# Kernel tuning notes

Measured on AMD Instinct MI355X. Metric: run time of the kernel, lower is better.

## Reference

```python
import jax, jax.numpy as jnp
import numpy as np

PAD = 4
B, C, H, W = 64, 9, 256, 256


def setup_inputs() -> dict:
    key = jax.random.key(0)
    k1, k2, k3 = jax.random.split(key, 3)
    x = jax.random.normal(k1, (B, C, H, W), dtype=jnp.float32)
    shift_x = jax.random.randint(k2, (B,), 0, 2 * PAD + 1, dtype=jnp.int32)
    shift_y = jax.random.randint(k3, (B,), 0, 2 * PAD + 1, dtype=jnp.int32)
    return {"x": x, "shift_x": shift_x, "shift_y": shift_y}


def _lerp_gather(xp, idx_f, axis_size, axis):
    """Separable bilinear tap along one spatial axis with zeros padding.

    xp: (B, C, D2, D3); idx_f: (B, L) fractional pixel indices along `axis`.
    Returns gathered+interpolated tensor with that axis resized to L.
    """
    i0 = jnp.floor(idx_f)
    w1 = idx_f - i0
    w0 = 1.0 - w1
    i1 = i0 + 1.0

    def tap(i, w):
        valid = (i >= 0) & (i <= axis_size - 1)  # zeros padding_mode
        ic = jnp.clip(i, 0, axis_size - 1).astype(jnp.int32)
        wm = w * valid
        if axis == 3:
            g = jnp.take_along_axis(xp, ic[:, None, None, :], axis=3)
            return g * wm[:, None, None, :]
        else:
            g = jnp.take_along_axis(xp, ic[:, None, :, None], axis=2)
            return g * wm[:, None, :, None]

    return tap(i0, w0) + tap(i1, w1)


def reference(x, shift_x, shift_y):
    b, c, h, w = x.shape
    p = PAD
    hp, wp = h + 2 * p, w + 2 * p
    # replicate pad
    x_pad = jnp.pad(x, ((0, 0), (0, 0), (p, p), (p, p)), mode='edge')
    # base grid (normalized coords, H/W points spanning [-1+eps, 1-eps])
    eps_h, eps_w = 2.0 / hp, 2.0 / wp
    gy = jnp.linspace(-1.0 + eps_h, 1.0 - eps_h, h).astype(x.dtype)  # (H,)
    gx = jnp.linspace(-1.0 + eps_w, 1.0 - eps_w, w).astype(x.dtype)  # (W,)
    # per-sample integer-pixel shift in normalized units
    gxb = gx[None, :] + shift_x.astype(x.dtype)[:, None] * (2.0 / wp)  # (B,W)
    gyb = gy[None, :] + shift_y.astype(x.dtype)[:, None] * (2.0 / hp)  # (B,H)
    # normalized -> pixel coords (align_corners=False)
    ix = ((gxb + 1.0) * wp - 1.0) * 0.5  # (B,W)
    iy = ((gyb + 1.0) * hp - 1.0) * 0.5  # (B,H)
    # separable bilinear grid_sample with zeros padding
    tmp = _lerp_gather(x_pad, ix, wp, axis=3)  # (B,C,Hp,W)
    out = _lerp_gather(tmp, iy, hp, axis=2)    # (B,C,H,W)
    return out
```

## Files before the change

kernel.cpp:

```cpp
#include <hip/hip_runtime.h>

#define PAD 4
#define B_ 64
#define C_ 9
#define H_ 256
#define W_ 256
#define PEXT 264
#define TILE_R 16
#define SROWS 18
#define LROW 268
#define NBLK (B_ * C_ * (H_ / TILE_R))

__global__ __launch_bounds__(256) void RandomShiftsAug_kernel(
    const float* __restrict__ x,
    const int* __restrict__ shift_x,
    const int* __restrict__ shift_y,
    float* __restrict__ out)
{
    __shared__ float sm[SROWS * LROW];

    const int tid  = threadIdx.x;
    const int lane = tid & 63;
    const int wv   = tid >> 6;

    const int wid  = (blockIdx.x & 7) * (NBLK / 8) + (blockIdx.x >> 3);

    const int bc   = wid >> 4;
    const int rblk = wid & 15;
    const int i0   = rblk << 4;
    const int b    = bc / C_;

    const float STEP = 262.0f / 255.0f;
    const float sx = (float)shift_x[b];
    const float sy = (float)shift_y[b];
    const float xbase = 0.5f + sx;
    const float ybase = 0.5f + sy;

    const int sr_base = (int)floorf(fmaf((float)i0, STEP, ybase));
    const int sr_last = (int)floorf(fmaf((float)(i0 + TILE_R - 1), STEP, ybase)) + 1;
    const int srows   = sr_last - sr_base + 1;

    const float* __restrict__ plane = x + (size_t)bc * (size_t)(H_ * W_);

    for (int s = wv; s < srows; s += 4) {
        const int rs = min(max(sr_base + s - PAD, 0), H_ - 1);
        const float* src = plane + rs * W_ + lane * 4;
        float* dst = &sm[s * LROW + 4];
        __builtin_amdgcn_global_load_lds(
            (const __attribute__((address_space(1))) void*)src,
            (__attribute__((address_space(3))) void*)dst,
            16, 0, 0);
    }

    if (tid < srows * 9) {
        const int s = tid / 9;
        const int e = tid - s * 9;
        const int rs = min(max(sr_base + s - PAD, 0), H_ - 1);
        const int p    = (e < 4) ? e : (256 + e);
        const int srcc = (e < 4) ? 0 : (W_ - 1);
        sm[s * LROW + p] = plane[rs * W_ + srcc];
    }
    __syncthreads();

    float wx0[4], wx1[4];
    int rdc[4];
    #pragma unroll
    for (int c = 0; c < 4; ++c) {
        const int j   = lane + 64 * c;
        const float ixv = fmaf((float)j, STEP, xbase);
        const float fx  = floorf(ixv);
        const int   px0 = (int)fx;
        float w1 = ixv - fx;
        float w0 = 1.0f - w1;
        if (px0 > PEXT - 1)     w0 = 0.0f;
        if (px0 + 1 > PEXT - 1) w1 = 0.0f;
        wx0[c] = w0;
        wx1[c] = w1;
        rdc[c] = min(px0, PEXT - 1);
    }

    #pragma unroll
    for (int m = 0; m < 4; ++m) {
        const int i = i0 + wv * 4 + m;
        const float iyv = fmaf((float)i, STEP, ybase);
        const float fy  = floorf(iyv);
        const int   py0 = (int)fy;
        float wy1 = iyv - fy;
        float wy0 = 1.0f - wy1;
        if (py0 > PEXT - 1)     wy0 = 0.0f;
        if (py0 + 1 > PEXT - 1) wy1 = 0.0f;
        const int s0 = py0 - sr_base;
        const float* __restrict__ r0p = &sm[s0 * LROW];
        const float* __restrict__ r1p = r0p + LROW;
        float* __restrict__ orow = out + ((size_t)(bc * H_ + i)) * (size_t)W_;

        #pragma unroll
        for (int c = 0; c < 4; ++c) {
            const int rd = rdc[c];
            const float v00 = r0p[rd], v01 = r0p[rd + 1];
            const float v10 = r1p[rd], v11 = r1p[rd + 1];
            const float a0 = fmaf(v00, wx0[c], v01 * wx1[c]);
            const float a1 = fmaf(v10, wx0[c], v11 * wx1[c]);
            orow[lane + 64 * c] = fmaf(a0, wy0, a1 * wy1);
        }
    }
}

extern "C" void kernel_launch(void* const* d_in, const int* in_sizes, int n_in,
                              void* d_out, int out_size, void* d_ws, size_t ws_size,
                              hipStream_t stream) {
    const float* x       = (const float*)d_in[0];
    const int*   shift_x = (const int*)d_in[1];
    const int*   shift_y = (const int*)d_in[2];
    float*       out     = (float*)d_out;

    RandomShiftsAug_kernel<<<NBLK, 256, 0, stream>>>(x, shift_x, shift_y, out);
}
```

Measured before the change: 52.35 us.

## Drop padded LDS halo, fold edge clamping into weights, store float2 outputs

Shared memory rows now hold only the 256 real columns, so the extra scalar pass that filled the replicate-pad halo is removed. The edge behaviour is rebuilt by clamping the column index and moving the weight onto the surviving tap. Each lane now handles two adjacent output columns and writes them with a float2 store. The barrier is placed after the per-column weight setup so that setup overlaps the async global-to-LDS loads. Risks include LDS bank conflicts from the stride-2 column pattern and possible mistakes in the edge weight folding.

```diff
diff --git a/kernel.cpp b/kernel.cpp
--- a/kernel.cpp
+++ b/kernel.cpp
@@ -8,7 +8,6 @@
 #define PEXT 264
 #define TILE_R 16
 #define SROWS 18
-#define LROW 268
 #define NBLK (B_ * C_ * (H_ / TILE_R))
 
 __global__ __launch_bounds__(256) void RandomShiftsAug_kernel(
@@ -17,7 +16,7 @@
     const int* __restrict__ shift_y,
     float* __restrict__ out)
 {
-    __shared__ float sm[SROWS * LROW];
+    __shared__ float sm[SROWS][W_];
 
     const int tid  = threadIdx.x;
     const int lane = tid & 63;
@@ -26,8 +25,7 @@
     const int wid  = (blockIdx.x & 7) * (NBLK / 8) + (blockIdx.x >> 3);
 
     const int bc   = wid >> 4;
-    const int rblk = wid & 15;
-    const int i0   = rblk << 4;
+    const int i0   = (wid & 15) << 4;
     const int b    = bc / C_;
 
     const float STEP = 262.0f / 255.0f;
@@ -36,37 +34,26 @@
     const float xbase = 0.5f + sx;
     const float ybase = 0.5f + sy;
 
+    const float* __restrict__ plane = x + (size_t)bc * (size_t)(H_ * W_);
+
     const int sr_base = (int)floorf(fmaf((float)i0, STEP, ybase));
-    const int sr_last = (int)floorf(fmaf((float)(i0 + TILE_R - 1), STEP, ybase)) + 1;
-    const int srows   = sr_last - sr_base + 1;
-
-    const float* __restrict__ plane = x + (size_t)bc * (size_t)(H_ * W_);
+    const int srows   = (int)floorf(fmaf((float)(i0 + TILE_R - 1), STEP, ybase))
+                        + 2 - sr_base;
 
     for (int s = wv; s < srows; s += 4) {
         const int rs = min(max(sr_base + s - PAD, 0), H_ - 1);
         const float* src = plane + rs * W_ + lane * 4;
-        float* dst = &sm[s * LROW + 4];
         __builtin_amdgcn_global_load_lds(
             (const __attribute__((address_space(1))) void*)src,
-            (__attribute__((address_space(3))) void*)dst,
+            (__attribute__((address_space(3))) void*)&sm[s][0],
             16, 0, 0);
     }
 
-    if (tid < srows * 9) {
-        const int s = tid / 9;
-        const int e = tid - s * 9;
-        const int rs = min(max(sr_base + s - PAD, 0), H_ - 1);
-        const int p    = (e < 4) ? e : (256 + e);
-        const int srcc = (e < 4) ? 0 : (W_ - 1);
-        sm[s * LROW + p] = plane[rs * W_ + srcc];
-    }
-    __syncthreads();
-
     float wx0[4], wx1[4];
-    int rdc[4];
+    int cx[4];
     #pragma unroll
     for (int c = 0; c < 4; ++c) {
-        const int j   = lane + 64 * c;
+        const int j = 2 * lane + (c & 1) + 128 * (c >> 1);
         const float ixv = fmaf((float)j, STEP, xbase);
         const float fx  = floorf(ixv);
         const int   px0 = (int)fx;
@@ -74,10 +61,15 @@
         float w0 = 1.0f - w1;
         if (px0 > PEXT - 1)     w0 = 0.0f;
         if (px0 + 1 > PEXT - 1) w1 = 0.0f;
+        const int s = px0 - PAD;
+        if (s < 0)    { w0 += w1; w1 = 0.0f; }
+        if (s >= 255) { w1 += w0; w0 = 0.0f; }
+        cx[c]  = min(max(s, 0), 254);
         wx0[c] = w0;
         wx1[c] = w1;
-        rdc[c] = min(px0, PEXT - 1);
     }
+
+    __syncthreads();
 
     #pragma unroll
     for (int m = 0; m < 4; ++m) {
@@ -90,18 +82,29 @@
         if (py0 > PEXT - 1)     wy0 = 0.0f;
         if (py0 + 1 > PEXT - 1) wy1 = 0.0f;
         const int s0 = py0 - sr_base;
-        const float* __restrict__ r0p = &sm[s0 * LROW];
-        const float* __restrict__ r1p = r0p + LROW;
-        float* __restrict__ orow = out + ((size_t)(bc * H_ + i)) * (size_t)W_;
+        const float* __restrict__ r0p = &sm[s0][0];
+        const float* __restrict__ r1p = &sm[s0 + 1][0];
+        float2* __restrict__ orow2 =
+            (float2*)(out + ((size_t)(bc * H_ + i)) * (size_t)W_);
 
         #pragma unroll
-        for (int c = 0; c < 4; ++c) {
-            const int rd = rdc[c];
-            const float v00 = r0p[rd], v01 = r0p[rd + 1];
-            const float v10 = r1p[rd], v11 = r1p[rd + 1];
-            const float a0 = fmaf(v00, wx0[c], v01 * wx1[c]);
-            const float a1 = fmaf(v10, wx0[c], v11 * wx1[c]);
-            orow[lane + 64 * c] = fmaf(a0, wy0, a1 * wy1);
+        for (int p = 0; p < 2; ++p) {
+            const int c0 = 2 * p, c1 = 2 * p + 1;
+            const int rd0 = cx[c0], rd1 = cx[c1];
+            const float v00 = r0p[rd0], v01 = r0p[rd0 + 1];
+            const float v02 = r0p[rd1], v03 = r0p[rd1 + 1];
+            const float v10 = r1p[rd0], v11 = r1p[rd0 + 1];
+            const float v12 = r1p[rd1], v13 = r1p[rd1 + 1];
+
+            const float a0 = fmaf(v00, wx0[c0], v01 * wx1[c0]);
+            const float b0 = fmaf(v10, wx0[c0], v11 * wx1[c0]);
+            const float a1 = fmaf(v02, wx0[c1], v03 * wx1[c1]);
+            const float b1 = fmaf(v12, wx0[c1], v13 * wx1[c1]);
+
+            float2 o;
+            o.x = fmaf(a0, wy0, b0 * wy1);
+            o.y = fmaf(a1, wy0, b1 * wy1);
+            orow2[lane + 64 * p] = o;
         }
     }
 }
```

Result: no change. 51.45 us (-1.7%).
